# Optimization experiments

Measured on AMD Instinct MI355X. Metric: run time of the kernel, lower is better.

Reference implementation:

```python
import jax, jax.numpy as jnp
import numpy as np

B, T, H, E2, NPIX, CDIM, VOCAB = 8, 8, 512, 512, 49, 2048, 10000


def setup_inputs() -> dict:
    key = jax.random.key(0)
    ks = jax.random.split(key, 24)

    def w(k, shape, scale=0.02):
        return jax.random.normal(k, shape, jnp.float32) * scale

    return {
        "x": jax.random.normal(ks[0], (B, T, E2), jnp.float32),
        "hiddens": jax.random.normal(ks[1], (B, T, H), jnp.float32),
        "cells": jax.random.normal(ks[2], (B, T, H), jnp.float32),
        "V": jax.random.normal(ks[3], (B, NPIX, CDIM), jnp.float32),
        # Sentinel params
        "Wsx": w(ks[4], (E2, H)), "Wsh": w(ks[5], (H, H)),
        # Atten params (stored as [in, out]; Linear(in, out, bias=False))
        "Wv": w(ks[6], (CDIM, NPIX)), "Wg": w(ks[7], (H, NPIX)),
        "Ws": w(ks[8], (H, NPIX)), "Wh": w(ks[9], (NPIX, 1)),
        "Wfeat": w(ks[10], (1, 512)), "Wcxt": w(ks[11], (512, 1)),
        "Wg2": w(ks[12], (H, 512)), "Wspat": w(ks[13], (CDIM, 512)),
        "Wchan": w(ks[14], (NPIX, 512)),
        "Wgvs": w(ks[15], (H, 512)), "Wgvc": w(ks[16], (H, 512)),
        "Wghs": w(ks[17], (H, 512)), "Wghc": w(ks[18], (H, 512)),
        # Final classifier (has bias)
        "Wmlp": w(ks[19], (H, VOCAB)), "bmlp": jnp.zeros((VOCAB,), jnp.float32),
    }


def _forward(x, hiddens, cells, V, Wsx, Wsh, Wv, Wg, Ws, Wh, Wfeat, Wcxt,
             Wg2, Wspat, Wchan, Wgvs, Wgvc, Wghs, Wghc, Wmlp, bmlp):
    b, t, hdim = hiddens.shape
    # shifted hidden states: [h0, h_0..h_{T-2}]
    h0 = jnp.zeros((b, 1, hdim), hiddens.dtype)
    h_prev = jnp.concatenate([h0, hiddens[:, :-1, :]], axis=1) if t > 1 else h0
    # Sentinel: s_t = sigmoid(Wx x + Wh h_{t-1}) * tanh(cell)
    s = jax.nn.sigmoid(x @ Wsx + h_prev @ Wsh) * jnp.tanh(cells)
    h = hiddens

    # ---- channel attention (alpha0) ----
    featmean = jnp.mean(V, axis=1)[..., None]          # [B, 2048, 1]
    feature_vec = featmean @ Wfeat                      # [B, 2048, 512]
    cxt_ = jnp.tanh(feature_vec[:, None, :, :] + (h @ Wg2)[:, :, None, :])  # [B,T,2048,512]
    cxt = (cxt_ @ Wcxt)[..., 0]                         # [B, T, 2048]
    alpha0 = jax.nn.softmax(cxt, axis=-1)               # channel weights

    # ---- spatial attention (alpha_t) over channel-reweighted features ----
    wf = alpha0[:, :, None, :] * V[:, None, :, :]       # [B, T, 49, 2048]
    content_v = jnp.tanh(wf @ Wv + (h @ Wg)[:, :, None, :])  # [B, T, 49, 49]
    z_t = (jnp.tanh(content_v) @ Wh)[..., 0]            # [B, T, 49]
    alpha_t = jax.nn.softmax(z_t, axis=-1)

    c_spatial = jnp.einsum('btk,bkd->btd', alpha_t, V)  # [B, T, 2048]
    c_channel = jnp.mean(wf, axis=-1)                   # [B, T, 49]
    spatial_info = c_spatial @ Wspat                    # [B, T, 512]
    channel_info = c_channel @ Wchan                    # [B, T, 512]

    # ---- sentinel gates ----
    s_gate = jax.nn.sigmoid(s @ Wgvs + h @ Wghs)
    c_gate = jax.nn.sigmoid(s @ Wgvc + h @ Wghc)

    # ---- beta (sentinel vs visual) ----
    content_s = s @ Ws + h @ Wg                         # [B, T, 49]
    z_ext = jnp.tanh(content_s) @ Wh                    # [B, T, 1]
    extended = jnp.concatenate([z_t, z_ext], axis=-1)   # [B, T, 50]
    alpha_hat = jax.nn.softmax(extended, axis=-1)
    beta = alpha_hat[:, :, -1:]                         # [B, T, 1]

    c_hat = s_gate * spatial_info + c_gate * channel_info
    scores = (c_hat + h) @ Wmlp + bmlp                  # [B, T, VOCAB]
    return scores, alpha_t, beta


def reference(x, hiddens, cells, V, Wsx, Wsh, Wv, Wg, Ws, Wh, Wfeat, Wcxt,
              Wg2, Wspat, Wchan, Wgvs, Wgvc, Wghs, Wghc, Wmlp, bmlp):
    return _forward(x, hiddens, cells, V, Wsx, Wsh, Wv, Wg, Ws, Wh, Wfeat, Wcxt,
                    Wg2, Wspat, Wchan, Wgvs, Wgvc, Wghs, Wghc, Wmlp, bmlp)
```

## Files before the change

kernel.cpp:

```cpp
#include <hip/hip_runtime.h>

#define H 512
#define NTOK 64
#define NPIX 49
#define CDIM 2048
#define VOCAB 10000

#define WS_S      0
#define WS_FM     163840
#define WS_G2F    180224
#define WS_P1     212992
#define WS_P2     245760
#define WS_CCH    278528
#define WS_A0     331776
#define WS_CSPT   331776
#define WS_CHT    331776
#define WS_SG2S   462848
#define WS_GSPS   2035712
#define WS_MS     4132864
#define WS_SCS    6591488
#define WS_MF     9151488

#define OUT_ALPHA 640000
#define OUT_BETA  643136

typedef __attribute__((ext_vector_type(8))) short short8;
typedef __attribute__((ext_vector_type(4))) float floatx4;

__device__ __forceinline__ float rcp_fast(float x) {
#if __has_builtin(__builtin_amdgcn_rcpf)
  return __builtin_amdgcn_rcpf(x);
#else
  return 1.0f / x;
#endif
}
__device__ __forceinline__ float tanh_f(float x) {
  float e = __expf(2.0f * x);
  return 1.0f - 2.0f * rcp_fast(e + 1.0f);
}
__device__ __forceinline__ float sigmoid_f(float x) {
  return rcp_fast(1.0f + __expf(-x));
}
__device__ __forceinline__ short f2bf(float x) {
  union { float f; unsigned u; } un; un.f = x;
  unsigned r = un.u + 0x7FFFu + ((un.u >> 16) & 1u);
  return (short)(r >> 16);
}
__device__ __forceinline__ float bf2f(unsigned short h) {
  union { unsigned u; float f; } cv; cv.u = ((unsigned)h) << 16;
  return cv.f;
}

__global__ __launch_bounds__(256) void k_sg2(const float* __restrict__ Wsx,
    const float* __restrict__ Wsh, const float* __restrict__ Wg2,
    const float* __restrict__ x, const float* __restrict__ hid,
    const float* __restrict__ V, float* __restrict__ ws) {
  int bid = blockIdx.x, tid = threadIdx.x;
  if (bid < 384) {
    __shared__ float aT[32 * 20];
    int c2 = bid & 1, kc = (bid >> 1) & 15, z = bid >> 5;
    int st = z >> 2, n0 = (z & 3) * 16;
    int c = c2 * 256 + tid;
    int k0 = kc * 32;
    const float* W = (st == 0) ? Wsx : (st == 1) ? Wsh : Wg2;
    for (int i = tid; i < 512; i += 256) {
      int nn = i >> 5, kk = i & 31;
      int tok = n0 + nn;
      float v;
      if (st == 0)      v = x[tok * 512 + k0 + kk];
      else if (st == 1) v = (tok & 7) ? hid[(tok - 1) * 512 + k0 + kk] : 0.0f;
      else              v = hid[tok * 512 + k0 + kk];
      aT[kk * 20 + nn] = v;
    }
    __syncthreads();
    float acc[16];
#pragma unroll
    for (int j = 0; j < 16; ++j) acc[j] = 0.0f;
#pragma unroll 4
    for (int kk = 0; kk < 32; ++kk) {
      float w = W[(k0 + kk) * 512 + c];
      const float4* a4 = (const float4*)&aT[kk * 20];
#pragma unroll
      for (int q = 0; q < 4; ++q) {
        float4 a = a4[q];
        acc[q * 4 + 0] += a.x * w;
        acc[q * 4 + 1] += a.y * w;
        acc[q * 4 + 2] += a.z * w;
        acc[q * 4 + 3] += a.w * w;
      }
    }
    float* C = ws + WS_SG2S + (st * 16 + kc) * 32768;
#pragma unroll
    for (int j = 0; j < 16; ++j) C[(n0 + j) * 512 + c] = acc[j];
  } else {
    int fb = bid - 384;
    int b = fb >> 3, c = (fb & 7) * 256 + tid;
    float s = 0.0f;
    for (int k = 0; k < NPIX; ++k) s += V[b * NPIX * CDIM + k * CDIM + c];
    ws[WS_FM + b * CDIM + c] = s * (1.0f / NPIX);
  }
}

__global__ __launch_bounds__(256) void k_act_s(const float* __restrict__ cells,
    float* __restrict__ ws) {
  int idx = blockIdx.x * 256 + threadIdx.x;
  float sa = 0.0f, g = 0.0f;
#pragma unroll
  for (int s = 0; s < 32; ++s) sa += ws[WS_SG2S + s * 32768 + idx];
#pragma unroll
  for (int s = 32; s < 48; ++s) g += ws[WS_SG2S + s * 32768 + idx];
  ws[WS_S + idx] = sigmoid_f(sa) * tanh_f(cells[idx]);
  ws[WS_G2F + idx] = g;
}

__global__ __launch_bounds__(256) void k_mid(const float* __restrict__ Wfeat,
    const float* __restrict__ Wcxt, const float* __restrict__ Wgvs,
    const float* __restrict__ Wghs, const float* __restrict__ Wgvc,
    const float* __restrict__ Wghc, const float* __restrict__ hid,
    const float* __restrict__ Wg, const float* __restrict__ Ws_,
    float* __restrict__ ws) {
  int bid = blockIdx.x, tid = threadIdx.x;
  if (bid < 512) {
    __shared__ float2 fw[512];
    __shared__ float g2l[512];
    int n = bid & 63, b = n >> 3;
    int c = (bid >> 6) * 256 + tid;
    for (int i = tid; i < 512; i += 256) {
      fw[i] = make_float2(Wfeat[i], Wcxt[i]);
      g2l[i] = ws[WS_G2F + n * H + i];
    }
    __syncthreads();
    float fm = ws[WS_FM + b * CDIM + c];
    float acc = 0.0f;
#pragma unroll 4
    for (int j = 0; j < 512; ++j) {
      float2 p = fw[j];
      acc += tanh_f(fm * p.x + g2l[j]) * p.y;
    }
    ws[WS_A0 + n * CDIM + c] = acc;
  } else if (bid < 768) {
    __shared__ float aT[64 * 20];
    int gi = bid - 512;
    int c = (gi & 1) * 256 + tid;
    int rest = gi >> 1;
    int kc = rest & 7;
    int zz = rest >> 3;
    int st = zz >> 2, n0 = (zz & 3) * 16;
    int k0 = kc * 64;
    const float* Asrc = (st & 1) ? hid : (ws + WS_S);
    const float* W = (st == 0) ? Wgvs : (st == 1) ? Wghs : (st == 2) ? Wgvc : Wghc;
    for (int i = tid; i < 1024; i += 256) {
      int nn = i >> 6, kk = i & 63;
      aT[kk * 20 + nn] = Asrc[(n0 + nn) * 512 + k0 + kk];
    }
    __syncthreads();
    float acc[16];
#pragma unroll
    for (int j = 0; j < 16; ++j) acc[j] = 0.0f;
#pragma unroll 4
    for (int kk = 0; kk < 64; ++kk) {
      float w = W[(k0 + kk) * 512 + c];
      const float4* a4 = (const float4*)&aT[kk * 20];
#pragma unroll
      for (int q = 0; q < 4; ++q) {
        float4 a = a4[q];
        acc[q * 4 + 0] += a.x * w;
        acc[q * 4 + 1] += a.y * w;
        acc[q * 4 + 2] += a.z * w;
        acc[q * 4 + 3] += a.w * w;
      }
    }
    float* C = ws + WS_GSPS + (st * 8 + kc) * 32768;
#pragma unroll
    for (int j = 0; j < 16; ++j) C[(n0 + j) * 512 + c] = acc[j];
  } else {
    int bidx = bid - 768;
    int n = bidx & 63, half = bidx >> 6;
    int k2 = tid & 63, w = tid >> 6;
    int kc = half * 4 + w;
    const float* hrow = hid + n * H;
    const float* srow = ws + WS_S + n * H;
    float a1 = 0.0f, a2 = 0.0f;
#pragma unroll 4
    for (int kk = 0; kk < 64; ++kk) {
      int k = kc * 64 + kk;
      if (k2 < NPIX) {
        a1 += hrow[k] * Wg[k * NPIX + k2];
        a2 += srow[k] * Ws_[k * NPIX + k2];
      }
    }
    if (k2 < NPIX) {
      ws[WS_P1 + (kc * 64 + n) * 64 + k2] = a1;
      ws[WS_P2 + (kc * 64 + n) * 64 + k2] = a2;
    }
  }
}

__global__ __launch_bounds__(256) void k_attnM(const float* __restrict__ V,
    const float* __restrict__ Wv, float* __restrict__ ws) {
  __shared__ __align__(16) short al[64 * 136];
  __shared__ __align__(16) short bl[64 * 136];
  __shared__ float red[8];
  int tid = threadIdx.x, bid = blockIdx.x;
  int kc = bid >> 6, n = bid & 63, b = n >> 3;
  int c0 = kc * 128;
  const float* cr = ws + WS_A0 + n * CDIM;
  const float* Vb = V + b * NPIX * CDIM + c0;
  int lane = tid & 63, w = tid >> 6;
  float v[8];
  float vmax = -1e30f;
#pragma unroll
  for (int i = 0; i < 8; ++i) { v[i] = cr[tid + i * 256]; vmax = fmaxf(vmax, v[i]); }
  for (int off = 32; off; off >>= 1) vmax = fmaxf(vmax, __shfl_xor(vmax, off));
  if (lane == 0) red[w] = vmax;
  __syncthreads();
  float m = fmaxf(fmaxf(red[0], red[1]), fmaxf(red[2], red[3]));
  float ss = 0.0f;
#pragma unroll
  for (int i = 0; i < 8; ++i) ss += __expf(v[i] - m);
  for (int off = 32; off; off >>= 1) ss += __shfl_xor(ss, off);
  if (lane == 0) red[4 + w] = ss;
  __syncthreads();
  float inv = rcp_fast(red[4] + red[5] + red[6] + red[7]);
  {
    int cc = tid & 127;
    float a0c = __expf(cr[c0 + cc] - m) * inv;
    for (int k = tid >> 7; k < NPIX; k += 2)
      al[k * 136 + cc] = f2bf(a0c * Vb[k * CDIM + cc]);
  }
  for (int idx = tid; idx < 128 * 64; idx += 256) {
    int cc = idx >> 6, r = idx & 63;
    if (r < NPIX) bl[r * 136 + cc] = f2bf(Wv[(c0 + cc) * NPIX + r]);
  }
  __syncthreads();
  if (tid < NPIX) {
    float cch = 0.0f;
    const unsigned short* ar = (const unsigned short*)(al + tid * 136);
#pragma unroll 8
    for (int cc = 0; cc < 128; ++cc) cch += bf2f(ar[cc]);
    ws[WS_CCH + (kc * 64 + n) * 52 + tid] = cch * (1.0f / CDIM);
  }
  int qm = lane >> 4, mr = lane & 15;
  floatx4 acc[4];
#pragma unroll
  for (int i = 0; i < 4; ++i) acc[i] = (floatx4){0.f, 0.f, 0.f, 0.f};
#pragma unroll
  for (int ks = 0; ks < 4; ++ks) {
    int cb = ks * 32 + qm * 8;
    short8 bf = *(const short8*)&bl[(w * 16 + mr) * 136 + cb];
#pragma unroll
    for (int i = 0; i < 4; ++i) {
      short8 af = *(const short8*)&al[(i * 16 + mr) * 136 + cb];
      acc[i] = __builtin_amdgcn_mfma_f32_16x16x32_bf16(af, bf, acc[i], 0, 0, 0);
    }
  }
  __syncthreads();
  float* ml = (float*)al;
  int k2 = w * 16 + mr;
  if (k2 < NPIX) {
#pragma unroll
    for (int i = 0; i < 4; ++i) {
#pragma unroll
      for (int r = 0; r < 4; ++r) {
        int kp = i * 16 + qm * 4 + r;
        if (kp < NPIX) ml[k2 * 49 + kp] = acc[i][r];
      }
    }
  }
  __syncthreads();
  float* Mp = ws + WS_MS + kc * 153664 + n * 2401;
  for (int idx = tid; idx < 2401; idx += 256) Mp[idx] = ml[idx];
}

__global__ __launch_bounds__(256) void k_redM(float* __restrict__ ws) {
  int n = blockIdx.y;
  int i = blockIdx.x * 256 + threadIdx.x;
  if (i < 2401) {
    float m = 0.0f;
#pragma unroll
    for (int s = 0; s < 16; ++s) m += ws[WS_MS + s * 153664 + n * 2401 + i];
    ws[WS_MF + n * 2401 + i] = m;
  }
}

__global__ __launch_bounds__(256) void k_zt(const float* __restrict__ Wh,
    float* __restrict__ ws, float* __restrict__ out) {
  __shared__ float gl[NPIX], cl[NPIX], whl[64];
  __shared__ float zbuf[4][64];
  int n = blockIdx.x, tid = threadIdx.x;
  if (tid < NPIX) {
    float s1 = 0.0f, s2 = 0.0f;
#pragma unroll
    for (int kc = 0; kc < 8; ++kc) {
      s1 += ws[WS_P1 + (kc * 64 + n) * 64 + tid];
      s2 += ws[WS_P2 + (kc * 64 + n) * 64 + tid];
    }
    gl[tid] = s1;
    cl[tid] = s1 + s2;
    whl[tid] = Wh[tid];
  }
  __syncthreads();
  int k = tid & 63, g = tid >> 6;
  float zp = 0.0f;
  if (k < NPIX) {
    int k2e = (g == 3) ? NPIX : (g * 13 + 13);
    const float* Mz = ws + WS_MF + n * 2401;
    for (int k2 = g * 13; k2 < k2e; ++k2) {
      float m = Mz[k2 * 49 + k];
      zp += tanh_f(tanh_f(m + gl[k2])) * whl[k2];
    }
  }
  zbuf[g][k] = zp;
  __syncthreads();
  if (tid < 64) {
    int lane = tid;
    float z = zbuf[0][lane] + zbuf[1][lane] + zbuf[2][lane] + zbuf[3][lane];
    float zm = (lane < NPIX) ? z : -1e30f;
    float m1 = zm;
    for (int off = 32; off; off >>= 1) m1 = fmaxf(m1, __shfl_xor(m1, off));
    float e = (lane < NPIX) ? __expf(z - m1) : 0.0f;
    float S1 = e;
    for (int off = 32; off; off >>= 1) S1 += __shfl_xor(S1, off);
    if (lane < NPIX) out[OUT_ALPHA + n * NPIX + lane] = e * rcp_fast(S1);
    float vz = (lane < NPIX) ? tanh_f(cl[lane]) * whl[lane] : 0.0f;
    for (int off = 32; off; off >>= 1) vz += __shfl_xor(vz, off);
    if (lane == 0) {
      float ze = vz;
      float m2 = fmaxf(m1, ze);
      float S2 = S1 * __expf(m1 - m2) + __expf(ze - m2);
      out[OUT_BETA + n] = __expf(ze - m2) * rcp_fast(S2);
    }
  }
}

__global__ __launch_bounds__(256) void k_cspatial(const float* __restrict__ V,
    const float* __restrict__ out, float* __restrict__ ws) {
  __shared__ float al[NPIX];
  int bid = blockIdx.x, tid = threadIdx.x;
  int n = bid & 63, b = n >> 3;
  int d = (bid >> 6) * 256 + tid;
  if (tid < NPIX) al[tid] = out[OUT_ALPHA + n * NPIX + tid];
  __syncthreads();
  float s = 0.0f;
#pragma unroll 7
  for (int k = 0; k < NPIX; ++k) s += al[k] * V[b * NPIX * CDIM + k * CDIM + d];
  ws[WS_CSPT + d * 64 + n] = s;
}

__global__ __launch_bounds__(256) void k_gemm_spat(const float* __restrict__ Wspat,
    float* __restrict__ ws) {
  int c = blockIdx.x * 256 + threadIdx.x;
  int kc = blockIdx.y;
  int z = blockIdx.z;
  int st = 4 + (z >> 2), n0 = (z & 3) * 16;
  int q = st - 4;
  const float* A = ws + WS_CSPT + q * 32768;
  const float* W = Wspat + q * 262144;
  int k0 = kc * 64;
  float acc[16];
#pragma unroll
  for (int j = 0; j < 16; ++j) acc[j] = 0.0f;
#pragma unroll 4
  for (int kk = 0; kk < 64; ++kk) {
    int k = k0 + kk;
    float w = W[k * 512 + c];
    const float4* A4 = (const float4*)(A + k * 64 + n0);
#pragma unroll
    for (int q2 = 0; q2 < 4; ++q2) {
      float4 a = A4[q2];
      acc[q2 * 4 + 0] += a.x * w;
      acc[q2 * 4 + 1] += a.y * w;
      acc[q2 * 4 + 2] += a.z * w;
      acc[q2 * 4 + 3] += a.w * w;
    }
  }
  float* C = ws + WS_GSPS + (st * 8 + kc) * 32768;
#pragma unroll
  for (int j = 0; j < 16; ++j) C[(n0 + j) * 512 + c] = acc[j];
}

__global__ __launch_bounds__(256) void k_chat(const float* __restrict__ hid,
    const float* __restrict__ Wchan, float* __restrict__ ws) {
  __shared__ float cl[NPIX];
  int tid = threadIdx.x, n = blockIdx.y;
  int c = blockIdx.x * 256 + tid;
  if (tid < NPIX) {
    float s = 0.0f;
#pragma unroll
    for (int kc = 0; kc < 16; ++kc) s += ws[WS_CCH + (kc * 64 + n) * 52 + tid];
    cl[tid] = s;
  }
  __syncthreads();
  float acc = 0.0f;
#pragma unroll 7
  for (int k = 0; k < NPIX; ++k) acc += cl[k] * Wchan[k * H + c];
  int idx = n * H + c;
  float ga1 = 0.0f, ga2 = 0.0f, spat = 0.0f;
#pragma unroll
  for (int s = 0; s < 16; ++s)  ga1 += ws[WS_GSPS + s * 32768 + idx];
#pragma unroll
  for (int s = 16; s < 32; ++s) ga2 += ws[WS_GSPS + s * 32768 + idx];
#pragma unroll
  for (int s = 32; s < 64; ++s) spat += ws[WS_GSPS + s * 32768 + idx];
  float chat = sigmoid_f(ga1) * spat + sigmoid_f(ga2) * acc + hid[idx];
  ((short*)(ws + WS_CHT))[idx] = f2bf(chat);
}

__global__ __launch_bounds__(256) void k_gemm_scores(const float* __restrict__ Wmlp,
    float* __restrict__ ws) {
  __shared__ __align__(16) short bl[64 * 136];
  int tid = threadIdx.x;
  int cb = blockIdx.x, kc = blockIdx.y;
  int c0 = cb * 64, k0 = kc * 128;
  const short* CHB = (const short*)(ws + WS_CHT);
  int lane = tid & 63, w = tid >> 6;
  int mr = lane & 15, kg = lane >> 4;
  for (int i = tid; i < 128 * 64; i += 256) {
    int kk = i >> 6, cc = i & 63;
    int c = c0 + cc;
    float v = (c < VOCAB) ? Wmlp[(k0 + kk) * VOCAB + c] : 0.0f;
    bl[cc * 136 + kk] = f2bf(v);
  }
  __syncthreads();
  floatx4 acc[4];
#pragma unroll
  for (int i = 0; i < 4; ++i) acc[i] = (floatx4){0.f, 0.f, 0.f, 0.f};
#pragma unroll
  for (int ks = 0; ks < 4; ++ks) {
    short8 af = *(const short8*)&CHB[(w * 16 + mr) * 512 + k0 + ks * 32 + kg * 8];
#pragma unroll
    for (int ct = 0; ct < 4; ++ct) {
      short8 bf = *(const short8*)&bl[(ct * 16 + mr) * 136 + ks * 32 + kg * 8];
      acc[ct] = __builtin_amdgcn_mfma_f32_16x16x32_bf16(af, bf, acc[ct], 0, 0, 0);
    }
  }
  float* slab = ws + WS_SCS + kc * 640000;
#pragma unroll
  for (int ct = 0; ct < 4; ++ct) {
    int c = c0 + ct * 16 + mr;
    if (c < VOCAB) {
#pragma unroll
      for (int r = 0; r < 4; ++r) {
        int n = w * 16 + kg * 4 + r;
        slab[n * VOCAB + c] = acc[ct][r];
      }
    }
  }
}

__global__ __launch_bounds__(256) void k_red_scores(const float* __restrict__ bmlp,
    float* __restrict__ ws, float* __restrict__ out) {
  int c4 = blockIdx.x * 256 + threadIdx.x, n = blockIdx.y;
  if (c4 >= VOCAB / 4) return;
  const float4* b4 = (const float4*)bmlp;
  float4 v = b4[c4];
#pragma unroll
  for (int s = 0; s < 4; ++s) {
    float4 p = ((const float4*)(ws + WS_SCS + s * 640000 + n * VOCAB))[c4];
    v.x += p.x; v.y += p.y; v.z += p.z; v.w += p.w;
  }
  ((float4*)(out + n * VOCAB))[c4] = v;
}

extern "C" void kernel_launch(void* const* d_in, const int* in_sizes, int n_in,
                              void* d_out, int out_size, void* d_ws, size_t ws_size,
                              hipStream_t stream) {
  const float* x     = (const float*)d_in[0];
  const float* hid   = (const float*)d_in[1];
  const float* cells = (const float*)d_in[2];
  const float* V     = (const float*)d_in[3];
  const float* Wsx   = (const float*)d_in[4];
  const float* Wsh   = (const float*)d_in[5];
  const float* Wv    = (const float*)d_in[6];
  const float* Wg    = (const float*)d_in[7];
  const float* Ws_   = (const float*)d_in[8];
  const float* Wh    = (const float*)d_in[9];
  const float* Wfeat = (const float*)d_in[10];
  const float* Wcxt  = (const float*)d_in[11];
  const float* Wg2   = (const float*)d_in[12];
  const float* Wspat = (const float*)d_in[13];
  const float* Wchan = (const float*)d_in[14];
  const float* Wgvs  = (const float*)d_in[15];
  const float* Wgvc  = (const float*)d_in[16];
  const float* Wghs  = (const float*)d_in[17];
  const float* Wghc  = (const float*)d_in[18];
  const float* Wmlp  = (const float*)d_in[19];
  const float* bmlp  = (const float*)d_in[20];
  float* ws  = (float*)d_ws;
  float* out = (float*)d_out;

  hipLaunchKernelGGL(k_sg2, dim3(448), dim3(256), 0, stream, Wsx, Wsh, Wg2, x, hid, V, ws);
  hipLaunchKernelGGL(k_act_s, dim3(128), dim3(256), 0, stream, cells, ws);
  hipLaunchKernelGGL(k_mid, dim3(896), dim3(256), 0, stream, Wfeat, Wcxt, Wgvs, Wghs, Wgvc, Wghc, hid, Wg, Ws_, ws);
  hipLaunchKernelGGL(k_attnM, dim3(1024), dim3(256), 0, stream, V, Wv, ws);
  hipLaunchKernelGGL(k_redM, dim3(10, 64), dim3(256), 0, stream, ws);
  hipLaunchKernelGGL(k_zt, dim3(64), dim3(256), 0, stream, Wh, ws, out);
  hipLaunchKernelGGL(k_cspatial, dim3(512), dim3(256), 0, stream, V, out, ws);
  hipLaunchKernelGGL(k_gemm_spat, dim3(2, 8, 16), dim3(256), 0, stream, Wspat, ws);
  hipLaunchKernelGGL(k_chat, dim3(2, 64), dim3(256), 0, stream, hid, Wchan, ws);
  hipLaunchKernelGGL(k_gemm_scores, dim3(157, 4), dim3(256), 0, stream, Wmlp, ws);
  hipLaunchKernelGGL(k_red_scores, dim3(10, 64), dim3(256), 0, stream, bmlp, ws, out);
}
```

Measured before the change: 221.2 us.

## Fuse spatial context into Wspat GEMM and drop split-K score reduction

Merges the alpha-weighted spatial reduction over V into the Wspat GEMM kernel. The fused kernel computes its 64-channel by 16-token slice of the spatial context in shared memory instead of writing it to workspace and reading it back. The score GEMM now loops over all K chunks in one block and adds the bias directly, which removes the split-K slabs and the separate reduction kernel. This saves two launches and the workspace round trips. In exchange, the spatial context is recomputed redundantly across the two column blocks, and the score GEMM runs only 157 blocks with serialized K, so it has less parallelism.

```diff
diff --git a/kernel.cpp b/kernel.cpp
--- a/kernel.cpp
+++ b/kernel.cpp
@@ -13,12 +13,10 @@
 #define WS_P2     245760
 #define WS_CCH    278528
 #define WS_A0     331776
-#define WS_CSPT   331776
 #define WS_CHT    331776
 #define WS_SG2S   462848
 #define WS_GSPS   2035712
 #define WS_MS     4132864
-#define WS_SCS    6591488
 #define WS_MF     9151488
 
 #define OUT_ALPHA 640000
@@ -333,48 +331,64 @@
   }
 }
 
-__global__ __launch_bounds__(256) void k_cspatial(const float* __restrict__ V,
-    const float* __restrict__ out, float* __restrict__ ws) {
-  __shared__ float al[NPIX];
-  int bid = blockIdx.x, tid = threadIdx.x;
-  int n = bid & 63, b = n >> 3;
-  int d = (bid >> 6) * 256 + tid;
-  if (tid < NPIX) al[tid] = out[OUT_ALPHA + n * NPIX + tid];
-  __syncthreads();
-  float s = 0.0f;
+__global__ __launch_bounds__(256) void k_cspat(const float* __restrict__ V,
+    const float* __restrict__ Wspat, const float* __restrict__ out,
+    float* __restrict__ ws) {
+  __shared__ float vs[2 * 49 * 64];
+  __shared__ float alp[16 * 64];
+  __shared__ float aT[64 * 20];
+  int tid = threadIdx.x;
+  int c2 = blockIdx.x, kc = blockIdx.y, z = blockIdx.z;
+  int q = z >> 2, n0 = (z & 3) * 16;
+  int d0 = q * 512 + kc * 64;
+  int b0 = n0 >> 3;
+  for (int i = tid; i < 2 * 49 * 64; i += 256) {
+    int d = i & 63, t = i >> 6;
+    int bb = (t >= 49) ? 1 : 0;
+    int kp = t - bb * 49;
+    vs[i] = V[(b0 + bb) * NPIX * CDIM + kp * CDIM + d0 + d];
+  }
+  for (int i = tid; i < 1024; i += 256) {
+    int nl = i >> 6, kp = i & 63;
+    alp[i] = (kp < NPIX) ? out[OUT_ALPHA + (n0 + nl) * NPIX + kp] : 0.0f;
+  }
+  __syncthreads();
+  {
+    int d = tid & 63, ng = tid >> 6;
+    int bb = ng >> 1;
+    float a0 = 0.f, a1 = 0.f, a2 = 0.f, a3 = 0.f;
 #pragma unroll 7
-  for (int k = 0; k < NPIX; ++k) s += al[k] * V[b * NPIX * CDIM + k * CDIM + d];
-  ws[WS_CSPT + d * 64 + n] = s;
-}
-
-__global__ __launch_bounds__(256) void k_gemm_spat(const float* __restrict__ Wspat,
-    float* __restrict__ ws) {
-  int c = blockIdx.x * 256 + threadIdx.x;
-  int kc = blockIdx.y;
-  int z = blockIdx.z;
-  int st = 4 + (z >> 2), n0 = (z & 3) * 16;
-  int q = st - 4;
-  const float* A = ws + WS_CSPT + q * 32768;
-  const float* W = Wspat + q * 262144;
-  int k0 = kc * 64;
+    for (int kp = 0; kp < NPIX; ++kp) {
+      float v = vs[(bb * 49 + kp) * 64 + d];
+      a0 += alp[(ng * 4 + 0) * 64 + kp] * v;
+      a1 += alp[(ng * 4 + 1) * 64 + kp] * v;
+      a2 += alp[(ng * 4 + 2) * 64 + kp] * v;
+      a3 += alp[(ng * 4 + 3) * 64 + kp] * v;
+    }
+    aT[d * 20 + ng * 4 + 0] = a0;
+    aT[d * 20 + ng * 4 + 1] = a1;
+    aT[d * 20 + ng * 4 + 2] = a2;
+    aT[d * 20 + ng * 4 + 3] = a3;
+  }
+  __syncthreads();
+  int c = c2 * 256 + tid;
   float acc[16];
 #pragma unroll
   for (int j = 0; j < 16; ++j) acc[j] = 0.0f;
 #pragma unroll 4
   for (int kk = 0; kk < 64; ++kk) {
-    int k = k0 + kk;
-    float w = W[k * 512 + c];
-    const float4* A4 = (const float4*)(A + k * 64 + n0);
+    float w = Wspat[(d0 + kk) * 512 + c];
+    const float4* a4 = (const float4*)&aT[kk * 20];
 #pragma unroll
     for (int q2 = 0; q2 < 4; ++q2) {
-      float4 a = A4[q2];
+      float4 a = a4[q2];
       acc[q2 * 4 + 0] += a.x * w;
       acc[q2 * 4 + 1] += a.y * w;
       acc[q2 * 4 + 2] += a.z * w;
       acc[q2 * 4 + 3] += a.w * w;
     }
   }
-  float* C = ws + WS_GSPS + (st * 8 + kc) * 32768;
+  float* C = ws + WS_GSPS + ((4 + q) * 8 + kc) * 32768;
 #pragma unroll
   for (int j = 0; j < 16; ++j) C[(n0 + j) * 512 + c] = acc[j];
 }
@@ -407,59 +421,51 @@
 }
 
 __global__ __launch_bounds__(256) void k_gemm_scores(const float* __restrict__ Wmlp,
-    float* __restrict__ ws) {
+    const float* __restrict__ bmlp, float* __restrict__ ws,
+    float* __restrict__ out) {
   __shared__ __align__(16) short bl[64 * 136];
   int tid = threadIdx.x;
-  int cb = blockIdx.x, kc = blockIdx.y;
-  int c0 = cb * 64, k0 = kc * 128;
+  int cb = blockIdx.x;
+  int c0 = cb * 64;
   const short* CHB = (const short*)(ws + WS_CHT);
   int lane = tid & 63, w = tid >> 6;
   int mr = lane & 15, kg = lane >> 4;
-  for (int i = tid; i < 128 * 64; i += 256) {
-    int kk = i >> 6, cc = i & 63;
-    int c = c0 + cc;
-    float v = (c < VOCAB) ? Wmlp[(k0 + kk) * VOCAB + c] : 0.0f;
-    bl[cc * 136 + kk] = f2bf(v);
-  }
-  __syncthreads();
   floatx4 acc[4];
 #pragma unroll
   for (int i = 0; i < 4; ++i) acc[i] = (floatx4){0.f, 0.f, 0.f, 0.f};
 #pragma unroll
-  for (int ks = 0; ks < 4; ++ks) {
-    short8 af = *(const short8*)&CHB[(w * 16 + mr) * 512 + k0 + ks * 32 + kg * 8];
-#pragma unroll
-    for (int ct = 0; ct < 4; ++ct) {
-      short8 bf = *(const short8*)&bl[(ct * 16 + mr) * 136 + ks * 32 + kg * 8];
-      acc[ct] = __builtin_amdgcn_mfma_f32_16x16x32_bf16(af, bf, acc[ct], 0, 0, 0);
-    }
-  }
-  float* slab = ws + WS_SCS + kc * 640000;
+  for (int s = 0; s < 4; ++s) {
+    int k0 = s * 128;
+    __syncthreads();
+    for (int i = tid; i < 128 * 64; i += 256) {
+      int kk = i >> 6, cc = i & 63;
+      int c = c0 + cc;
+      float v = (c < VOCAB) ? Wmlp[(k0 + kk) * VOCAB + c] : 0.0f;
+      bl[cc * 136 + kk] = f2bf(v);
+    }
+    __syncthreads();
+#pragma unroll
+    for (int ks = 0; ks < 4; ++ks) {
+      short8 af = *(const short8*)&CHB[(w * 16 + mr) * 512 + k0 + ks * 32 + kg * 8];
+#pragma unroll
+      for (int ct = 0; ct < 4; ++ct) {
+        short8 bf = *(const short8*)&bl[(ct * 16 + mr) * 136 + ks * 32 + kg * 8];
+        acc[ct] = __builtin_amdgcn_mfma_f32_16x16x32_bf16(af, bf, acc[ct], 0, 0, 0);
+      }
+    }
+  }
 #pragma unroll
   for (int ct = 0; ct < 4; ++ct) {
     int c = c0 + ct * 16 + mr;
     if (c < VOCAB) {
+      float bv = bmlp[c];
 #pragma unroll
       for (int r = 0; r < 4; ++r) {
         int n = w * 16 + kg * 4 + r;
-        slab[n * VOCAB + c] = acc[ct][r];
+        out[n * VOCAB + c] = acc[ct][r] + bv;
       }
     }
   }
-}
-
-__global__ __launch_bounds__(256) void k_red_scores(const float* __restrict__ bmlp,
-    float* __restrict__ ws, float* __restrict__ out) {
-  int c4 = blockIdx.x * 256 + threadIdx.x, n = blockIdx.y;
-  if (c4 >= VOCAB / 4) return;
-  const float4* b4 = (const float4*)bmlp;
-  float4 v = b4[c4];
-#pragma unroll
-  for (int s = 0; s < 4; ++s) {
-    float4 p = ((const float4*)(ws + WS_SCS + s * 640000 + n * VOCAB))[c4];
-    v.x += p.x; v.y += p.y; v.z += p.z; v.w += p.w;
-  }
-  ((float4*)(out + n * VOCAB))[c4] = v;
 }
 
 extern "C" void kernel_launch(void* const* d_in, const int* in_sizes, int n_in,
@@ -495,9 +501,7 @@
   hipLaunchKernelGGL(k_attnM, dim3(1024), dim3(256), 0, stream, V, Wv, ws);
   hipLaunchKernelGGL(k_redM, dim3(10, 64), dim3(256), 0, stream, ws);
   hipLaunchKernelGGL(k_zt, dim3(64), dim3(256), 0, stream, Wh, ws, out);
-  hipLaunchKernelGGL(k_cspatial, dim3(512), dim3(256), 0, stream, V, out, ws);
-  hipLaunchKernelGGL(k_gemm_spat, dim3(2, 8, 16), dim3(256), 0, stream, Wspat, ws);
+  hipLaunchKernelGGL(k_cspat, dim3(2, 8, 16), dim3(256), 0, stream, V, Wspat, out, ws);
   hipLaunchKernelGGL(k_chat, dim3(2, 64), dim3(256), 0, stream, hid, Wchan, ws);
-  hipLaunchKernelGGL(k_gemm_scores, dim3(157, 4), dim3(256), 0, stream, Wmlp, ws);
-  hipLaunchKernelGGL(k_red_scores, dim3(10, 64), dim3(256), 0, stream, bmlp, ws, out);
-}
+  hipLaunchKernelGGL(k_gemm_scores, dim3(157), dim3(256), 0, stream, Wmlp, bmlp, ws, out);
+}
```

After: 245.9 us. +11.2%, slower.
